# Optimization experiments

Measured on AMD Instinct MI355X. Metric: run time of the kernel, lower is better.

The kernel has to match this reference:

```python
import jax, jax.numpy as jnp
import numpy as np

B, P_DIM, H_DIM, X_DIM = 4096, 1024, 2048, 1024


def setup_inputs() -> dict:
    key = jax.random.key(0)
    ks = jax.random.split(key, 24)
    def lin_w(k, out_d, in_d):
        bound = 1.0 / np.sqrt(in_d)
        return jax.random.uniform(k, (out_d, in_d), jnp.float32, -bound, bound)
    def lin_b(k, out_d, in_d):
        bound = 1.0 / np.sqrt(in_d)
        return jax.random.uniform(k, (out_d,), jnp.float32, -bound, bound)
    inp = {
        "P": jax.random.normal(ks[0], (B, P_DIM), jnp.float32),
        "hidden": jax.random.normal(ks[1], (B, H_DIM), jnp.float32),
        "cell": jax.random.normal(ks[2], (B, H_DIM), jnp.float32),
        "ext_input": jax.random.normal(ks[3], (B, X_DIM), jnp.float32),
        "W_pi": lin_w(ks[4], H_DIM, P_DIM), "b_pi": lin_b(ks[5], H_DIM, P_DIM),
        "W_pf": lin_w(ks[6], H_DIM, P_DIM), "b_pf": lin_b(ks[7], H_DIM, P_DIM),
        "W_pg": lin_w(ks[8], H_DIM, P_DIM), "b_pg": lin_b(ks[9], H_DIM, P_DIM),
        "W_po": lin_w(ks[10], H_DIM, P_DIM), "b_po": lin_b(ks[11], H_DIM, P_DIM),
        "W_hi": lin_w(ks[12], H_DIM, H_DIM), "W_hf": lin_w(ks[13], H_DIM, H_DIM),
        "W_hg": lin_w(ks[14], H_DIM, H_DIM), "W_ho": lin_w(ks[15], H_DIM, H_DIM),
        "W_xi": lin_w(ks[16], H_DIM, X_DIM), "W_xf": lin_w(ks[17], H_DIM, X_DIM),
        "W_xg": lin_w(ks[18], H_DIM, X_DIM), "W_xo": lin_w(ks[19], H_DIM, X_DIM),
    }
    return inp


def reference(P, hidden, cell, ext_input,
              W_pi, b_pi, W_pf, b_pf, W_pg, b_pg, W_po, b_po,
              W_hi, W_hf, W_hg, W_ho,
              W_xi, W_xf, W_xg, W_xo):
    # Concatenate the 4 per-gate weights along the output axis -> 3 big GEMMs
    # (mathematically identical to the 12 separate nn.Linear calls).
    Wp = jnp.concatenate([W_pi, W_pf, W_pg, W_po], axis=0)   # [4H, P]
    bp = jnp.concatenate([b_pi, b_pf, b_pg, b_po], axis=0)   # [4H]
    Wh = jnp.concatenate([W_hi, W_hf, W_hg, W_ho], axis=0)   # [4H, H]
    Wx = jnp.concatenate([W_xi, W_xf, W_xg, W_xo], axis=0)   # [4H, X]
    gates = P @ Wp.T + bp + hidden @ Wh.T + ext_input @ Wx.T  # [B, 4H]
    gi, gf, gg, go = jnp.split(gates, 4, axis=-1)
    i = jax.nn.sigmoid(gi)
    f = jax.nn.sigmoid(gf)
    g = jnp.tanh(gg)
    o = jax.nn.sigmoid(go)
    c_new = f * cell + i * g
    h_new = o * jnp.tanh(c_new)
    return (h_new, c_new)
```

## Files before the change

### kernel.cpp

```cpp
#include <hip/hip_runtime.h>
#include <hip/hip_bf16.h>
#include <stdint.h>

#define B_DIM 4096
#define P_DIMC 1024
#define H_DIMC 2048
#define X_DIMC 1024
#define K_DIM 4096
#define N_DIM 8192

#define BM 256
#define BN 256
#define BK 32
#define NT (K_DIM / BK)

typedef __attribute__((ext_vector_type(8))) short bf16x8;
typedef __attribute__((ext_vector_type(4))) float f32x4;

__device__ __forceinline__ unsigned short f2bf(float f) {
  union { float f; unsigned u; } v; v.f = f;
  unsigned u = v.u;
  u += 0x7FFFu + ((u >> 16) & 1u);
  return (unsigned short)(u >> 16);
}

__device__ __forceinline__ float sigm(float x) { return 1.f / (1.f + __expf(-x)); }
__device__ __forceinline__ float tanh_fast(float x) {
  float e = __expf(2.f * x);
  return 1.f - 2.f / (e + 1.f);
}

__device__ __forceinline__ void gl_lds16(const void* g, void* l) {
  __builtin_amdgcn_global_load_lds((const __attribute__((address_space(1))) void*)g,
                                   (__attribute__((address_space(3))) void*)l, 16, 0, 0);
}

__global__ void pack_a_kernel(const float* __restrict__ P, const float* __restrict__ Hd,
                              const float* __restrict__ X, unsigned short* __restrict__ A) {
  const int total = B_DIM * (K_DIM / 4);
  for (int idx = blockIdx.x * blockDim.x + threadIdx.x; idx < total;
       idx += gridDim.x * blockDim.x) {
    int row = idx >> 10;
    int col = (idx & 1023) << 2;
    const float* src; int off;
    if (col < P_DIMC)                { src = P;  off = row * P_DIMC + col; }
    else if (col < P_DIMC + H_DIMC)  { src = Hd; off = row * H_DIMC + (col - P_DIMC); }
    else                             { src = X;  off = row * X_DIMC + (col - P_DIMC - H_DIMC); }
    float4 v = *(const float4*)(src + off);
    ushort4 o;
    o.x = f2bf(v.x); o.y = f2bf(v.y); o.z = f2bf(v.z); o.w = f2bf(v.w);
    *(ushort4*)(A + (size_t)row * K_DIM + col) = o;
  }
}

struct WPtrs {
  const float *pi, *pf, *pg, *po;
  const float *hi, *hf, *hg, *ho;
  const float *xi, *xf, *xg, *xo;
};

__global__ void pack_w_kernel(WPtrs w, unsigned short* __restrict__ Wo) {
  const int total = N_DIM * (K_DIM / 4);
  for (int idx = blockIdx.x * blockDim.x + threadIdx.x; idx < total;
       idx += gridDim.x * blockDim.x) {
    int n = idx >> 10;
    int col = (idx & 1023) << 2;
    int gate = (n >> 4) & 3;
    int h = ((n >> 6) << 4) | (n & 15);
    const float* src; int off;
    if (col < P_DIMC) {
      src = gate == 0 ? w.pi : gate == 1 ? w.pf : gate == 2 ? w.pg : w.po;
      off = h * P_DIMC + col;
    } else if (col < P_DIMC + H_DIMC) {
      src = gate == 0 ? w.hi : gate == 1 ? w.hf : gate == 2 ? w.hg : w.ho;
      off = h * H_DIMC + (col - P_DIMC);
    } else {
      src = gate == 0 ? w.xi : gate == 1 ? w.xf : gate == 2 ? w.xg : w.xo;
      off = h * X_DIMC + (col - P_DIMC - H_DIMC);
    }
    float4 v = *(const float4*)(src + off);
    ushort4 o;
    o.x = f2bf(v.x); o.y = f2bf(v.y); o.z = f2bf(v.z); o.w = f2bf(v.w);
    *(ushort4*)(Wo + (size_t)n * K_DIM + col) = o;
  }
}

__global__ __launch_bounds__(512, 1) void gemm_lstm_kernel(
    const unsigned short* __restrict__ A, const unsigned short* __restrict__ W,
    const float* __restrict__ cell,
    const float* __restrict__ bpi, const float* __restrict__ bpf,
    const float* __restrict__ bpg, const float* __restrict__ bpo,
    float* __restrict__ out) {
  __shared__ __align__(16) short As[4][BM * BK];
  __shared__ __align__(16) short Bs[4][BN * BK];

  const int T = threadIdx.x;
  const int wave = T >> 6, lane = T & 63;
  const int wm = wave >> 2, wn = wave & 3;

  const int x = blockIdx.x & 7, local = blockIdx.x >> 3;
  const int bm = (x & 1) * 8 + (local >> 3);
  const int bn = (x >> 1) * 8 + (local & 7);

  const int cg = ((T & 3) - (T >> 3)) & 3;
  const int rowS = T >> 2;
  const unsigned short* aG0 = A + (size_t)(bm * BM + rowS) * K_DIM + cg * 8;
  const unsigned short* aG1 = A + (size_t)(bm * BM + 128 + rowS) * K_DIM + cg * 8;
  const unsigned short* bG0 = W + (size_t)(bn * BN + rowS) * K_DIM + cg * 8;
  const unsigned short* bG1 = W + (size_t)(bn * BN + 128 + rowS) * K_DIM + cg * 8;
  const int dstOff = T * 8;

  const int lrow = lane & 15, kgrp = lane >> 4;
  const int slotR = (kgrp + (lrow >> 1)) & 3;
  int offA[8], offB[4];
#pragma unroll
  for (int mf = 0; mf < 8; ++mf) offA[mf] = (wm * 128 + mf * 16 + lrow) * BK + slotR * 8;
#pragma unroll
  for (int nf = 0; nf < 4; ++nf) offB[nf] = (wn * 64 + nf * 16 + lrow) * BK + slotR * 8;

  f32x4 acc[8][4] = {};

#pragma unroll
  for (int u = 0; u < 3; ++u) {
    short* dA = &As[u][0];
    short* dB = &Bs[u][0];
    const int kt = u * BK;
    gl_lds16(aG0 + kt, dA + dstOff);
    gl_lds16(aG1 + kt, dA + 4096 + dstOff);
    gl_lds16(bG0 + kt, dB + dstOff);
    gl_lds16(bG1 + kt, dB + 4096 + dstOff);
  }
  asm volatile("s_waitcnt vmcnt(8)" ::: "memory");
  __builtin_amdgcn_s_barrier();

  for (int t = 0; t < NT; ++t) {
    const short* bufA = &As[t & 3][0];
    const short* bufB = &Bs[t & 3][0];

    if (t < NT - 3) {
      const int kt = (t + 3) * BK;
      short* dA = &As[(t + 3) & 3][0];
      short* dB = &Bs[(t + 3) & 3][0];
      gl_lds16(aG0 + kt, dA + dstOff);
      gl_lds16(aG1 + kt, dA + 4096 + dstOff);
      gl_lds16(bG0 + kt, dB + dstOff);
      gl_lds16(bG1 + kt, dB + 4096 + dstOff);
    }

    bf16x8 av[8], bv[4];
#pragma unroll
    for (int i = 0; i < 4; ++i) bv[i] = *(const bf16x8*)(bufB + offB[i]);
#pragma unroll
    for (int i = 0; i < 8; ++i) av[i] = *(const bf16x8*)(bufA + offA[i]);

    __builtin_amdgcn_s_setprio(1);
#pragma unroll
    for (int mi = 0; mi < 8; ++mi)
#pragma unroll
      for (int ni = 0; ni < 4; ++ni)
        acc[mi][ni] = __builtin_amdgcn_mfma_f32_16x16x32_bf16(av[mi], bv[ni], acc[mi][ni], 0, 0, 0);
    __builtin_amdgcn_s_setprio(0);

    if (t < NT - 3)       { asm volatile("s_waitcnt vmcnt(8)" ::: "memory"); }
    else if (t == NT - 3) { asm volatile("s_waitcnt vmcnt(4)" ::: "memory"); }
    else if (t == NT - 2) { asm volatile("s_waitcnt vmcnt(0)" ::: "memory"); }
    __builtin_amdgcn_s_barrier();
  }

  const int h = bn * 64 + wn * 16 + lrow;
  const float bi = bpi[h], bf_ = bpf[h], bg = bpg[h], bo = bpo[h];
  const int rbase = bm * BM + wm * 128 + kgrp * 4;
#pragma unroll
  for (int mf = 0; mf < 8; ++mf) {
#pragma unroll
    for (int r = 0; r < 4; ++r) {
      const int brow = rbase + mf * 16 + r;
      float gi = acc[mf][0][r] + bi;
      float gf = acc[mf][1][r] + bf_;
      float gg = acc[mf][2][r] + bg;
      float go = acc[mf][3][r] + bo;
      float i_ = sigm(gi), f_ = sigm(gf), g_ = tanh_fast(gg), o_ = sigm(go);
      float cold = cell[(size_t)brow * H_DIMC + h];
      float cn = f_ * cold + i_ * g_;
      out[(size_t)brow * H_DIMC + h] = o_ * tanh_fast(cn);
      out[(size_t)B_DIM * H_DIMC + (size_t)brow * H_DIMC + h] = cn;
    }
  }
}

extern "C" void kernel_launch(void* const* d_in, const int* in_sizes, int n_in,
                              void* d_out, int out_size, void* d_ws, size_t ws_size,
                              hipStream_t stream) {
  const float* P    = (const float*)d_in[0];
  const float* Hd   = (const float*)d_in[1];
  const float* cell = (const float*)d_in[2];
  const float* X    = (const float*)d_in[3];
  WPtrs w;
  w.pi = (const float*)d_in[4];   const float* bpi = (const float*)d_in[5];
  w.pf = (const float*)d_in[6];   const float* bpf = (const float*)d_in[7];
  w.pg = (const float*)d_in[8];   const float* bpg = (const float*)d_in[9];
  w.po = (const float*)d_in[10];  const float* bpo = (const float*)d_in[11];
  w.hi = (const float*)d_in[12];  w.hf = (const float*)d_in[13];
  w.hg = (const float*)d_in[14];  w.ho = (const float*)d_in[15];
  w.xi = (const float*)d_in[16];  w.xf = (const float*)d_in[17];
  w.xg = (const float*)d_in[18];  w.xo = (const float*)d_in[19];

  unsigned short* Abf = (unsigned short*)d_ws;
  unsigned short* Wbf = Abf + (size_t)B_DIM * K_DIM;

  pack_a_kernel<<<2048, 256, 0, stream>>>(P, Hd, X, Abf);
  pack_w_kernel<<<2048, 256, 0, stream>>>(w, Wbf);
  gemm_lstm_kernel<<<512, 512, 0, stream>>>(Abf, Wbf, cell, bpi, bpf, bpg, bpo,
                                            (float*)d_out);
}
```

Before: 368.8 us.

## Restructure GEMM mainloop into four-phase ping-pong with BK=64 split-half LDS buffers

Doubles the K tile to 64 and replaces the 4-deep ring buffer with a double buffer split into A/B halves. Each K step is divided into four phases that interleave LDS reads, global-to-LDS staging and 16 MFMAs per phase, with barriers and waitcnts between phases. Wave-to-tile mapping and the weight packing permutation change so each wave's rows interleave at stride 32, and the epilogue is updated to match. The goal is better overlap of memory traffic with MFMA work and fewer loop iterations, at the cost of more barriers and a more fragile synchronisation scheme.

New measurement: 321.1 us. 1.15x faster.

```diff
diff --git a/kernel.cpp b/kernel.cpp
--- a/kernel.cpp
+++ b/kernel.cpp
@@ -11,7 +11,7 @@
 
 #define BM 256
 #define BN 256
-#define BK 32
+#define BK 64
 #define NT (K_DIM / BK)
 
 typedef __attribute__((ext_vector_type(8))) short bf16x8;
@@ -65,8 +65,8 @@
        idx += gridDim.x * blockDim.x) {
     int n = idx >> 10;
     int col = (idx & 1023) << 2;
-    int gate = (n >> 4) & 3;
-    int h = ((n >> 6) << 4) | (n & 15);
+    int gate = (n >> 6) & 3;
+    int h = (n >> 8) * 64 + ((n >> 4) & 3) * 16 + (n & 15);
     const float* src; int off;
     if (col < P_DIMC) {
       src = gate == 0 ? w.pi : gate == 1 ? w.pf : gate == 2 ? w.pg : w.po;
@@ -91,8 +91,8 @@
     const float* __restrict__ bpi, const float* __restrict__ bpf,
     const float* __restrict__ bpg, const float* __restrict__ bpo,
     float* __restrict__ out) {
-  __shared__ __align__(16) short As[4][BM * BK];
-  __shared__ __align__(16) short Bs[4][BN * BK];
+  __shared__ __align__(16) short As[2][2][8192];
+  __shared__ __align__(16) short Bs[2][2][8192];
 
   const int T = threadIdx.x;
   const int wave = T >> 6, lane = T & 63;
@@ -102,79 +102,108 @@
   const int bm = (x & 1) * 8 + (local >> 3);
   const int bn = (x >> 1) * 8 + (local & 7);
 
-  const int cg = ((T & 3) - (T >> 3)) & 3;
-  const int rowS = T >> 2;
-  const unsigned short* aG0 = A + (size_t)(bm * BM + rowS) * K_DIM + cg * 8;
-  const unsigned short* aG1 = A + (size_t)(bm * BM + 128 + rowS) * K_DIM + cg * 8;
-  const unsigned short* bG0 = W + (size_t)(bn * BN + rowS) * K_DIM + cg * 8;
-  const unsigned short* bG1 = W + (size_t)(bn * BN + 128 + rowS) * K_DIM + cg * 8;
-  const int dstOff = T * 8;
+  const int rA = T >> 3;
+  const int cg = ((T & 7) - (rA & 7)) & 7;
+  const unsigned short* aS0 = A + (size_t)(bm * BM + rA) * K_DIM + cg * 8;
+  const unsigned short* aS1 = A + (size_t)(bm * BM + 128 + rA) * K_DIM + cg * 8;
+  const unsigned short* bS0 = W + (size_t)(bn * BN + rA) * K_DIM + cg * 8;
+  const unsigned short* bS1 = W + (size_t)(bn * BN + 128 + rA) * K_DIM + cg * 8;
+  const int dOff = T * 8;
 
   const int lrow = lane & 15, kgrp = lane >> 4;
-  const int slotR = (kgrp + (lrow >> 1)) & 3;
-  int offA[8], offB[4];
-#pragma unroll
-  for (int mf = 0; mf < 8; ++mf) offA[mf] = (wm * 128 + mf * 16 + lrow) * BK + slotR * 8;
-#pragma unroll
-  for (int nf = 0; nf < 4; ++nf) offB[nf] = (wn * 64 + nf * 16 + lrow) * BK + slotR * 8;
+  const int aRow = (wm * 16 + lrow) * 64;
+  const int bRow = (wn * 16 + lrow) * 64;
+  const int sl0 = ((kgrp + (lrow & 7)) & 7) * 8;
+  const int sl1 = ((kgrp + 4 + (lrow & 7)) & 7) * 8;
 
   f32x4 acc[8][4] = {};
-
-#pragma unroll
-  for (int u = 0; u < 3; ++u) {
-    short* dA = &As[u][0];
-    short* dB = &Bs[u][0];
-    const int kt = u * BK;
-    gl_lds16(aG0 + kt, dA + dstOff);
-    gl_lds16(aG1 + kt, dA + 4096 + dstOff);
-    gl_lds16(bG0 + kt, dB + dstOff);
-    gl_lds16(bG1 + kt, dB + 4096 + dstOff);
-  }
-  asm volatile("s_waitcnt vmcnt(8)" ::: "memory");
+  bf16x8 ra[4][2], rb[2][2];
+
+  gl_lds16(aS0, &As[0][0][dOff]); gl_lds16(aS0 + (size_t)64 * K_DIM, &As[0][0][4096 + dOff]);
+  gl_lds16(bS0, &Bs[0][0][dOff]); gl_lds16(bS0 + (size_t)64 * K_DIM, &Bs[0][0][4096 + dOff]);
+  gl_lds16(aS1, &As[0][1][dOff]); gl_lds16(aS1 + (size_t)64 * K_DIM, &As[0][1][4096 + dOff]);
+  gl_lds16(bS1, &Bs[0][1][dOff]); gl_lds16(bS1 + (size_t)64 * K_DIM, &Bs[0][1][4096 + dOff]);
+  asm volatile("s_waitcnt vmcnt(4)" ::: "memory");
   __builtin_amdgcn_s_barrier();
 
+#define RD_A(HALF)                                                            \
+  _Pragma("unroll") for (int i = 0; i < 4; ++i) {                             \
+    ra[i][0] = *(const bf16x8*)(&As[cur][HALF][0] + aRow + i * 2048 + sl0);   \
+    ra[i][1] = *(const bf16x8*)(&As[cur][HALF][0] + aRow + i * 2048 + sl1);   \
+  }
+#define RD_B(HALF)                                                            \
+  _Pragma("unroll") for (int j = 0; j < 2; ++j) {                             \
+    rb[j][0] = *(const bf16x8*)(&Bs[cur][HALF][0] + bRow + j * 4096 + sl0);   \
+    rb[j][1] = *(const bf16x8*)(&Bs[cur][HALF][0] + bRow + j * 4096 + sl1);   \
+  }
+#define MFMA16(MH, NH)                                                        \
+  __builtin_amdgcn_s_setprio(1);                                              \
+  _Pragma("unroll") for (int i = 0; i < 4; ++i)                               \
+  _Pragma("unroll") for (int j = 0; j < 2; ++j) {                             \
+    acc[(MH)*4 + i][(NH)*2 + j] = __builtin_amdgcn_mfma_f32_16x16x32_bf16(    \
+        ra[i][0], rb[j][0], acc[(MH)*4 + i][(NH)*2 + j], 0, 0, 0);            \
+    acc[(MH)*4 + i][(NH)*2 + j] = __builtin_amdgcn_mfma_f32_16x16x32_bf16(    \
+        ra[i][1], rb[j][1], acc[(MH)*4 + i][(NH)*2 + j], 0, 0, 0);            \
+  }                                                                           \
+  __builtin_amdgcn_s_setprio(0);                                              \
+  __builtin_amdgcn_sched_barrier(0);
+#define FENCE_IN()                                                            \
+  __builtin_amdgcn_s_barrier();                                               \
+  asm volatile("s_waitcnt lgkmcnt(0)" ::: "memory");                          \
+  __builtin_amdgcn_sched_barrier(0);
+#define STAGE(SRC, DARR, NXT, HALF)                                           \
+  { const unsigned short* s_ = (SRC) + ktn * BK;                              \
+    gl_lds16(s_, &DARR[NXT][HALF][dOff]);                                     \
+    gl_lds16(s_ + (size_t)64 * K_DIM, &DARR[NXT][HALF][4096 + dOff]); }
+
   for (int t = 0; t < NT; ++t) {
-    const short* bufA = &As[t & 3][0];
-    const short* bufB = &Bs[t & 3][0];
-
-    if (t < NT - 3) {
-      const int kt = (t + 3) * BK;
-      short* dA = &As[(t + 3) & 3][0];
-      short* dB = &Bs[(t + 3) & 3][0];
-      gl_lds16(aG0 + kt, dA + dstOff);
-      gl_lds16(aG1 + kt, dA + 4096 + dstOff);
-      gl_lds16(bG0 + kt, dB + dstOff);
-      gl_lds16(bG1 + kt, dB + 4096 + dstOff);
-    }
-
-    bf16x8 av[8], bv[4];
-#pragma unroll
-    for (int i = 0; i < 4; ++i) bv[i] = *(const bf16x8*)(bufB + offB[i]);
-#pragma unroll
-    for (int i = 0; i < 8; ++i) av[i] = *(const bf16x8*)(bufA + offA[i]);
-
-    __builtin_amdgcn_s_setprio(1);
-#pragma unroll
-    for (int mi = 0; mi < 8; ++mi)
-#pragma unroll
-      for (int ni = 0; ni < 4; ++ni)
-        acc[mi][ni] = __builtin_amdgcn_mfma_f32_16x16x32_bf16(av[mi], bv[ni], acc[mi][ni], 0, 0, 0);
-    __builtin_amdgcn_s_setprio(0);
-
-    if (t < NT - 3)       { asm volatile("s_waitcnt vmcnt(8)" ::: "memory"); }
-    else if (t == NT - 3) { asm volatile("s_waitcnt vmcnt(4)" ::: "memory"); }
-    else if (t == NT - 2) { asm volatile("s_waitcnt vmcnt(0)" ::: "memory"); }
-    __builtin_amdgcn_s_barrier();
-  }
+    const int cur = t & 1, nxt = cur ^ 1;
+    const int ktn = t + 1;
+    const bool st = (t < NT - 1);
+
+    RD_A(0) RD_B(0)
+    if (st) STAGE(aS0, As, nxt, 0)
+    FENCE_IN()
+    MFMA16(0, 0)
+    if (st) { asm volatile("s_waitcnt vmcnt(4)" ::: "memory"); }
+    else    { asm volatile("s_waitcnt vmcnt(2)" ::: "memory"); }
+    __builtin_amdgcn_s_barrier();
+
+    RD_A(1)
+    if (st) STAGE(bS0, Bs, nxt, 0)
+    FENCE_IN()
+    MFMA16(1, 0)
+    if (st) { asm volatile("s_waitcnt vmcnt(4)" ::: "memory"); }
+    else    { asm volatile("s_waitcnt vmcnt(0)" ::: "memory"); }
+    __builtin_amdgcn_s_barrier();
+
+    RD_B(1)
+    if (st) STAGE(aS1, As, nxt, 1)
+    FENCE_IN()
+    MFMA16(1, 1)
+    __builtin_amdgcn_s_barrier();
+
+    RD_A(0)
+    if (st) STAGE(bS1, Bs, nxt, 1)
+    FENCE_IN()
+    MFMA16(0, 1)
+    if (st) { asm volatile("s_waitcnt vmcnt(4)" ::: "memory"); }
+    __builtin_amdgcn_s_barrier();
+  }
+#undef RD_A
+#undef RD_B
+#undef MFMA16
+#undef FENCE_IN
+#undef STAGE
 
   const int h = bn * 64 + wn * 16 + lrow;
   const float bi = bpi[h], bf_ = bpf[h], bg = bpg[h], bo = bpo[h];
-  const int rbase = bm * BM + wm * 128 + kgrp * 4;
+  const int rbase = bm * BM + wm * 16 + kgrp * 4;
 #pragma unroll
   for (int mf = 0; mf < 8; ++mf) {
 #pragma unroll
     for (int r = 0; r < 4; ++r) {
-      const int brow = rbase + mf * 16 + r;
+      const int brow = rbase + mf * 32 + r;
       float gi = acc[mf][0][r] + bi;
       float gf = acc[mf][1][r] + bf_;
       float gg = acc[mf][2][r] + bg;
```

## Restructure GEMM main loop into BK=64 four-phase double-buffered pipeline

Applied to the files above, without the earlier changes.

The K tile doubles from 32 to 64 and the 4-stage LDS ring becomes a double buffer split into two 128-row halves for A and B. Each K step now runs in four phases: each phase issues one half-tile global→LDS prefetch, loads a 4x4 fragment set from LDS, and runs 16 MFMAs between barriers and sched_barrier fences. B fragments are reused across consecutive phases. The aim is finer interleaving of loads, LDS reads and MFMA work with fewer registers live per phase. The cost is four block-wide barriers per K step and tighter waitcnt bookkeeping, so correctness and speed depend on the hand-tuned ordering.

After: 321.9 us. 12.7% less time.

```diff
diff --git a/kernel.cpp b/kernel.cpp
--- a/kernel.cpp
+++ b/kernel.cpp
@@ -11,7 +11,7 @@
 
 #define BM 256
 #define BN 256
-#define BK 32
+#define BK 64
 #define NT (K_DIM / BK)
 
 typedef __attribute__((ext_vector_type(8))) short bf16x8;
@@ -91,81 +91,122 @@
     const float* __restrict__ bpi, const float* __restrict__ bpf,
     const float* __restrict__ bpg, const float* __restrict__ bpo,
     float* __restrict__ out) {
-  __shared__ __align__(16) short As[4][BM * BK];
-  __shared__ __align__(16) short Bs[4][BN * BK];
+  __shared__ __align__(16) short As[2][2][8192];
+  __shared__ __align__(16) short Bs[2][2][8192];
 
   const int T = threadIdx.x;
   const int wave = T >> 6, lane = T & 63;
   const int wm = wave >> 2, wn = wave & 3;
+  const int wbh = wn >> 1;
 
   const int x = blockIdx.x & 7, local = blockIdx.x >> 3;
   const int bm = (x & 1) * 8 + (local >> 3);
   const int bn = (x >> 1) * 8 + (local & 7);
 
-  const int cg = ((T & 3) - (T >> 3)) & 3;
-  const int rowS = T >> 2;
-  const unsigned short* aG0 = A + (size_t)(bm * BM + rowS) * K_DIM + cg * 8;
-  const unsigned short* aG1 = A + (size_t)(bm * BM + 128 + rowS) * K_DIM + cg * 8;
-  const unsigned short* bG0 = W + (size_t)(bn * BN + rowS) * K_DIM + cg * 8;
-  const unsigned short* bG1 = W + (size_t)(bn * BN + 128 + rowS) * K_DIM + cg * 8;
-  const int dstOff = T * 8;
+  const int rS = T >> 3;
+  const int cg = ((T & 7) - (rS & 7)) & 7;
+  const unsigned short* aS0 = A + (size_t)(bm * BM + rS) * K_DIM + cg * 8;
+  const unsigned short* aS1 = A + (size_t)(bm * BM + 128 + rS) * K_DIM + cg * 8;
+  const unsigned short* bS0 = W + (size_t)(bn * BN + rS) * K_DIM + cg * 8;
+  const unsigned short* bS1 = W + (size_t)(bn * BN + 128 + rS) * K_DIM + cg * 8;
+  const int dOff = T * 8;
+
+#define STG(SRCP, KOFF, DSTBASE)                                              \
+  { const unsigned short* s_ = (SRCP) + (KOFF);                               \
+    gl_lds16(s_, (DSTBASE) + dOff);                                           \
+    gl_lds16(s_ + (size_t)64 * K_DIM, (DSTBASE) + 4096 + dOff); }
 
   const int lrow = lane & 15, kgrp = lane >> 4;
-  const int slotR = (kgrp + (lrow >> 1)) & 3;
-  int offA[8], offB[4];
-#pragma unroll
-  for (int mf = 0; mf < 8; ++mf) offA[mf] = (wm * 128 + mf * 16 + lrow) * BK + slotR * 8;
-#pragma unroll
-  for (int nf = 0; nf < 4; ++nf) offB[nf] = (wn * 64 + nf * 16 + lrow) * BK + slotR * 8;
+  const int rb = lrow & 7;
+  const int sk0 = ((kgrp + rb) & 7) * 8;
+  const int sk1 = ((kgrp + 4 + rb) & 7) * 8;
+  const int aRowB = lrow * 64;
+  const int bRowB = ((wn & 1) * 64 + lrow) * 64;
 
   f32x4 acc[8][4] = {};
-
-#pragma unroll
-  for (int u = 0; u < 3; ++u) {
-    short* dA = &As[u][0];
-    short* dB = &Bs[u][0];
-    const int kt = u * BK;
-    gl_lds16(aG0 + kt, dA + dstOff);
-    gl_lds16(aG1 + kt, dA + 4096 + dstOff);
-    gl_lds16(bG0 + kt, dB + dstOff);
-    gl_lds16(bG1 + kt, dB + 4096 + dstOff);
-  }
-  asm volatile("s_waitcnt vmcnt(8)" ::: "memory");
+  bf16x8 av[4], bv[4];
+
+  STG(bS0, 0, &Bs[0][0][0])
+  STG(bS1, 0, &Bs[0][1][0])
+  STG(aS0, 0, &As[0][0][0])
+  STG(aS1, 0, &As[0][1][0])
+  STG(bS0, BK, &Bs[1][0][0])
+  asm volatile("s_waitcnt vmcnt(2)" ::: "memory");
   __builtin_amdgcn_s_barrier();
 
+#define FENCE_PRE()                                                           \
+  __builtin_amdgcn_sched_barrier(0);                                          \
+  __builtin_amdgcn_s_barrier();                                               \
+  asm volatile("s_waitcnt lgkmcnt(0)" ::: "memory");                          \
+  __builtin_amdgcn_sched_barrier(0);
+#define FENCE_POST()                                                          \
+  __builtin_amdgcn_s_setprio(0);                                              \
+  __builtin_amdgcn_sched_barrier(0);                                          \
+  __builtin_amdgcn_s_barrier();
+
   for (int t = 0; t < NT; ++t) {
-    const short* bufA = &As[t & 3][0];
-    const short* bufB = &Bs[t & 3][0];
-
-    if (t < NT - 3) {
-      const int kt = (t + 3) * BK;
-      short* dA = &As[(t + 3) & 3][0];
-      short* dB = &Bs[(t + 3) & 3][0];
-      gl_lds16(aG0 + kt, dA + dstOff);
-      gl_lds16(aG1 + kt, dA + 4096 + dstOff);
-      gl_lds16(bG0 + kt, dB + dstOff);
-      gl_lds16(bG1 + kt, dB + 4096 + dstOff);
-    }
-
-    bf16x8 av[8], bv[4];
-#pragma unroll
-    for (int i = 0; i < 4; ++i) bv[i] = *(const bf16x8*)(bufB + offB[i]);
-#pragma unroll
-    for (int i = 0; i < 8; ++i) av[i] = *(const bf16x8*)(bufA + offA[i]);
-
-    __builtin_amdgcn_s_setprio(1);
-#pragma unroll
-    for (int mi = 0; mi < 8; ++mi)
-#pragma unroll
-      for (int ni = 0; ni < 4; ++ni)
-        acc[mi][ni] = __builtin_amdgcn_mfma_f32_16x16x32_bf16(av[mi], bv[ni], acc[mi][ni], 0, 0, 0);
-    __builtin_amdgcn_s_setprio(0);
-
-    if (t < NT - 3)       { asm volatile("s_waitcnt vmcnt(8)" ::: "memory"); }
-    else if (t == NT - 3) { asm volatile("s_waitcnt vmcnt(4)" ::: "memory"); }
-    else if (t == NT - 2) { asm volatile("s_waitcnt vmcnt(0)" ::: "memory"); }
-    __builtin_amdgcn_s_barrier();
-  }
+    const int cur = t & 1, nxt = cur ^ 1;
+    const short* A_w = &As[cur][wm][0];
+    const short* B_w = &Bs[cur][wbh][0];
+    const int k1 = (t + 1) * BK, k2 = (t + 2) * BK;
+
+#pragma unroll
+    for (int i = 0; i < 4; ++i) av[i] = *(const bf16x8*)(A_w + aRowB + i * 1024 + sk0);
+#pragma unroll
+    for (int j = 0; j < 4; ++j) bv[j] = *(const bf16x8*)(B_w + bRowB + j * 1024 + sk0);
+    if (t < NT - 1) STG(bS1, k1, &Bs[nxt][1][0])
+    if (t < NT - 1) { asm volatile("s_waitcnt vmcnt(4)" ::: "memory"); }
+    else            { asm volatile("s_waitcnt vmcnt(0)" ::: "memory"); }
+    FENCE_PRE()
+    __builtin_amdgcn_s_setprio(1);
+#pragma unroll
+    for (int i = 0; i < 4; ++i)
+#pragma unroll
+      for (int j = 0; j < 4; ++j)
+        acc[i][j] = __builtin_amdgcn_mfma_f32_16x16x32_bf16(av[i], bv[j], acc[i][j], 0, 0, 0);
+    FENCE_POST()
+
+#pragma unroll
+    for (int i = 0; i < 4; ++i) av[i] = *(const bf16x8*)(A_w + aRowB + (4 + i) * 1024 + sk0);
+    if (t < NT - 1) STG(aS0, k1, &As[nxt][0][0])
+    FENCE_PRE()
+    __builtin_amdgcn_s_setprio(1);
+#pragma unroll
+    for (int i = 0; i < 4; ++i)
+#pragma unroll
+      for (int j = 0; j < 4; ++j)
+        acc[4 + i][j] = __builtin_amdgcn_mfma_f32_16x16x32_bf16(av[i], bv[j], acc[4 + i][j], 0, 0, 0);
+    FENCE_POST()
+
+#pragma unroll
+    for (int i = 0; i < 4; ++i) av[i] = *(const bf16x8*)(A_w + aRowB + (4 + i) * 1024 + sk1);
+#pragma unroll
+    for (int j = 0; j < 4; ++j) bv[j] = *(const bf16x8*)(B_w + bRowB + j * 1024 + sk1);
+    if (t < NT - 1) STG(aS1, k1, &As[nxt][1][0])
+    FENCE_PRE()
+    __builtin_amdgcn_s_setprio(1);
+#pragma unroll
+    for (int i = 0; i < 4; ++i)
+#pragma unroll
+      for (int j = 0; j < 4; ++j)
+        acc[4 + i][j] = __builtin_amdgcn_mfma_f32_16x16x32_bf16(av[i], bv[j], acc[4 + i][j], 0, 0, 0);
+    FENCE_POST()
+
+#pragma unroll
+    for (int i = 0; i < 4; ++i) av[i] = *(const bf16x8*)(A_w + aRowB + i * 1024 + sk1);
+    if (t < NT - 2) STG(bS0, k2, &Bs[cur][0][0])
+    FENCE_PRE()
+    __builtin_amdgcn_s_setprio(1);
+#pragma unroll
+    for (int i = 0; i < 4; ++i)
+#pragma unroll
+      for (int j = 0; j < 4; ++j)
+        acc[i][j] = __builtin_amdgcn_mfma_f32_16x16x32_bf16(av[i], bv[j], acc[i][j], 0, 0, 0);
+    FENCE_POST()
+  }
+#undef STG
+#undef FENCE_PRE
+#undef FENCE_POST
 
   const int h = bn * 64 + wn * 16 + lrow;
   const float bi = bpi[h], bf_ = bpf[h], bg = bpg[h], bo = bpo[h];
```
